# Kernel optimization log

Hardware: AMD Instinct MI355X
Metric: run time of the kernel (lower is better)

## Reference

```python
import jax, jax.numpy as jnp
import numpy as np

K, N, F_IN, F_HID, F_OUT = 4, 8192, 128, 64, 16
DROPOUT_P = 0.3


def setup_inputs() -> dict:
    key = jax.random.key(0)
    ks = jax.random.split(key, 8)
    return {
        "adj": jax.random.uniform(ks[0], (K, N, N), dtype=jnp.float32),
        "x": jax.random.normal(ks[1], (N, F_IN), dtype=jnp.float32),
        "W1": jax.random.normal(ks[2], (F_IN, F_HID), dtype=jnp.float32) * 0.05,
        "b1": jax.random.normal(ks[3], (F_HID,), dtype=jnp.float32) * 0.05,
        "W2": jax.random.normal(ks[4], (F_HID, F_OUT), dtype=jnp.float32) * 0.05,
        "b2": jax.random.normal(ks[5], (F_OUT,), dtype=jnp.float32) * 0.05,
        "pi1": jax.random.normal(ks[6], (K,), dtype=jnp.float32),
        "pi2": jax.random.normal(ks[7], (K,), dtype=jnp.float32),
    }


def _gconv(adj, x, W, b, pi):
    # mixed adjacency: [N, N] = sum_k pi[k] * adj[k]
    A = jnp.einsum('k,knm->nm', pi, adj)
    support = x @ W                     # [N, F_out]
    return A @ support + b              # [N, F_out]


def reference(adj, x, W1, b1, W2, b2, pi1, pi2):
    # gc1.pi is softmax-normalized in Co_GCN.forward
    pi1_n = jax.nn.softmax(pi1)
    h = jax.nn.relu(_gconv(adj, x, W1, b1, pi1_n))   # [N, F_HID]
    # F.dropout with p=0.3, training=True (functional default): fixed-key mask
    keep = jax.random.bernoulli(jax.random.key(42), 1.0 - DROPOUT_P, h.shape)
    h = jnp.where(keep, h / (1.0 - DROPOUT_P), 0.0)
    out = _gconv(adj, h, W2, b2, pi2)                # [N, F_OUT]
    return out
```

## Files before the change

kernel.cpp:

```cpp
#include <hip/hip_runtime.h>
#include <stdint.h>

#define NN 8192
#define FIN 128
#define FH 64
#define FO 16
#define BM 64
#define BN 64
#define SPLIT1 4
#define NRANGE1 (NN / SPLIT1)
#define NCHUNK1 (NRANGE1 / BN)
#define SPLIT2 16
#define NRANGE2 (NN / SPLIT2)

typedef float    f32x4 __attribute__((ext_vector_type(4)));
typedef _Float16 f16x4 __attribute__((ext_vector_type(4)));
typedef _Float16 f16x8 __attribute__((ext_vector_type(8)));
typedef _Float16 h2    __attribute__((ext_vector_type(2)));

union U8 { f16x8 v; h2 p[4]; };

static __device__ __forceinline__ void fma4(float4& acc, float a, const float4 s) {
  acc.x = fmaf(a, s.x, acc.x);
  acc.y = fmaf(a, s.y, acc.y);
  acc.z = fmaf(a, s.z, acc.z);
  acc.w = fmaf(a, s.w, acc.w);
}

static __device__ __forceinline__ float dot2(h2 a, h2 b, float c) {
#if defined(__has_builtin)
#if __has_builtin(__builtin_amdgcn_fdot2)
  return __builtin_amdgcn_fdot2(a, b, c, false);
#else
  return c + (float)a.x * (float)b.x + (float)a.y * (float)b.y;
#endif
#else
  return c + (float)a.x * (float)b.x + (float)a.y * (float)b.y;
#endif
}

__global__ __launch_bounds__(256) void k_s1(const float* __restrict__ x,
                                            const float* __restrict__ W1,
                                            _Float16* __restrict__ S1p) {
  __shared__ float W1l[FIN * FH];
  __shared__ float xl[16][FIN + 4];
  __shared__ float hl[16][FH];
  const int t = threadIdx.x;
  const int n0 = blockIdx.x * 16;
  for (int i = t; i < FIN * FH / 4; i += 256)
    ((float4*)W1l)[i] = ((const float4*)W1)[i];
  for (int i = t; i < 16 * FIN; i += 256) {
    int r = i >> 7, c = i & (FIN - 1);
    xl[r][c] = x[(size_t)(n0 + r) * FIN + c];
  }
  __syncthreads();
  const int m = t >> 4;
  const int j0 = (t & 15) << 2;
  float4 acc = {0.f, 0.f, 0.f, 0.f};
#pragma unroll 8
  for (int k = 0; k < FIN; ++k) {
    float xv = xl[m][k];
    float4 w = *(const float4*)&W1l[k * FH + j0];
    fma4(acc, xv, w);
  }
  *(float4*)&hl[m][j0] = acc;
  __syncthreads();
  const int j = t & 63;
  const int g = t >> 6;
#pragma unroll
  for (int e = 0; e < 2; ++e) {
    const int np = g * 2 + e;
    h2 v;
    v.x = (_Float16)hl[np * 2 + 0][j];
    v.y = (_Float16)hl[np * 2 + 1][j];
    *(h2*)&S1p[(((size_t)(n0 >> 1) + np) * FH + j) * 2] = v;
  }
}

__global__ __launch_bounds__(256) void k_pass1_fused(const float* __restrict__ adj,
                                                     const _Float16* __restrict__ S1p,
                                                     const float* __restrict__ pi1,
                                                     const float* __restrict__ pi2,
                                                     float* __restrict__ hpart,
                                                     _Float16* __restrict__ A2h) {
  __shared__ h2 Alds[BN / 2][BM];
  __shared__ _Float16 S1l[BN / 2][FH][2];
  const int t = threadIdx.x;
  const int mb = blockIdx.x >> 2;
  const int sp = blockIdx.x & 3;

  float p0 = pi1[0], p1 = pi1[1], p2 = pi1[2], p3 = pi1[3];
  float mx = fmaxf(fmaxf(p0, p1), fmaxf(p2, p3));
  float e0 = expf(p0 - mx), e1 = expf(p1 - mx), e2 = expf(p2 - mx), e3 = expf(p3 - mx);
  float inv = 1.0f / (e0 + e1 + e2 + e3);
  const float w0 = e0 * inv, w1 = e1 * inv, w2 = e2 * inv, w3 = e3 * inv;
  const float v0 = pi2[0], v1 = pi2[1], v2 = pi2[2], v3 = pi2[3];

  const size_t NN2 = (size_t)NN * NN;
  const size_t row0 = (size_t)mb * BM;
  const int nbase = sp * NRANGE1;

  const int n4 = t & 15;
  const int ms = t >> 4;
  const int m0 = (t & 15) << 2;
  const int j0 = (t >> 4) << 2;

  f32x4 pf[4][4];
  f16x8 pfS[2];

  float4 acc0 = {0,0,0,0}, acc1 = {0,0,0,0}, acc2 = {0,0,0,0}, acc3 = {0,0,0,0};

  auto ISSUE = [&](int c) {
    const int n0 = nbase + c * BN;
#pragma unroll
    for (int p = 0; p < 4; ++p) {
      const float* g = adj + (row0 + (size_t)(ms + (p << 4))) * NN + (size_t)(n0 + (n4 << 2));
      pf[p][0] = __builtin_nontemporal_load((const f32x4*)g);
      pf[p][1] = __builtin_nontemporal_load((const f32x4*)(g + NN2));
      pf[p][2] = __builtin_nontemporal_load((const f32x4*)(g + 2 * NN2));
      pf[p][3] = __builtin_nontemporal_load((const f32x4*)(g + 3 * NN2));
    }
    const f16x8* src = (const f16x8*)(S1p + (size_t)(n0 >> 1) * FH * 2);
    pfS[0] = src[t];
    pfS[1] = src[t + 256];
  };

  auto STAGE = [&](int c) {
    const int n0 = nbase + c * BN;
#pragma unroll
    for (int p = 0; p < 4; ++p) {
      const int ml = ms + (p << 4);
      f32x4 a0 = pf[p][0], a1 = pf[p][1], a2 = pf[p][2], a3 = pf[p][3];
      float c0 = fmaf(w0, a0.x, fmaf(w1, a1.x, fmaf(w2, a2.x, w3 * a3.x)));
      float c1 = fmaf(w0, a0.y, fmaf(w1, a1.y, fmaf(w2, a2.y, w3 * a3.y)));
      float c2 = fmaf(w0, a0.z, fmaf(w1, a1.z, fmaf(w2, a2.z, w3 * a3.z)));
      float c3 = fmaf(w0, a0.w, fmaf(w1, a1.w, fmaf(w2, a2.w, w3 * a3.w)));
      const int np0 = n4 * 2, np1 = np0 + 1;
      h2 u01; u01.x = (_Float16)c0; u01.y = (_Float16)c1;
      h2 u23; u23.x = (_Float16)c2; u23.y = (_Float16)c3;
      Alds[np0][ml ^ ((np0 & 7) << 2)] = u01;
      Alds[np1][ml ^ ((np1 & 7) << 2)] = u23;
      f16x4 h4;
      h4.x = (_Float16)fmaf(v0, a0.x, fmaf(v1, a1.x, fmaf(v2, a2.x, v3 * a3.x)));
      h4.y = (_Float16)fmaf(v0, a0.y, fmaf(v1, a1.y, fmaf(v2, a2.y, v3 * a3.y)));
      h4.z = (_Float16)fmaf(v0, a0.z, fmaf(v1, a1.z, fmaf(v2, a2.z, v3 * a3.z)));
      h4.w = (_Float16)fmaf(v0, a0.w, fmaf(v1, a1.w, fmaf(v2, a2.w, v3 * a3.w)));
      *(f16x4*)(A2h + (row0 + (size_t)ml) * NN + (size_t)(n0 + (n4 << 2))) = h4;
    }
    f16x8* dst = (f16x8*)&S1l[0][0][0];
    dst[t]       = pfS[0];
    dst[t + 256] = pfS[1];
  };

  ISSUE(0);
  for (int c = 0; c < NCHUNK1; ++c) {
    __syncthreads();
    STAGE(c);
    if (c + 1 < NCHUNK1) ISSUE(c + 1);
    asm volatile("s_waitcnt lgkmcnt(0)" ::: "memory");
    __builtin_amdgcn_s_barrier();
#pragma unroll 4
    for (int np = 0; np < BN / 2; ++np) {
      const int s = (np & 7) << 2;
      U8 a;  a.v  = *(const f16x8*)&Alds[np][m0 ^ s];
      U8 sv; sv.v = *(const f16x8*)&S1l[np][j0][0];
      acc0.x = dot2(a.p[0], sv.p[0], acc0.x);
      acc0.y = dot2(a.p[0], sv.p[1], acc0.y);
      acc0.z = dot2(a.p[0], sv.p[2], acc0.z);
      acc0.w = dot2(a.p[0], sv.p[3], acc0.w);
      acc1.x = dot2(a.p[1], sv.p[0], acc1.x);
      acc1.y = dot2(a.p[1], sv.p[1], acc1.y);
      acc1.z = dot2(a.p[1], sv.p[2], acc1.z);
      acc1.w = dot2(a.p[1], sv.p[3], acc1.w);
      acc2.x = dot2(a.p[2], sv.p[0], acc2.x);
      acc2.y = dot2(a.p[2], sv.p[1], acc2.y);
      acc2.z = dot2(a.p[2], sv.p[2], acc2.z);
      acc2.w = dot2(a.p[2], sv.p[3], acc2.w);
      acc3.x = dot2(a.p[3], sv.p[0], acc3.x);
      acc3.y = dot2(a.p[3], sv.p[1], acc3.y);
      acc3.z = dot2(a.p[3], sv.p[2], acc3.z);
      acc3.w = dot2(a.p[3], sv.p[3], acc3.w);
    }
  }
  float* hp = hpart + (size_t)sp * NN * FH;
  const size_t rbase = (row0 + m0) * FH + j0;
  *(float4*)&hp[rbase]          = acc0;
  *(float4*)&hp[rbase + FH]     = acc1;
  *(float4*)&hp[rbase + 2 * FH] = acc2;
  *(float4*)&hp[rbase + 3 * FH] = acc3;
}

__device__ __forceinline__ float dropout_scale(uint32_t e) {
  uint32_t x0 = 0u;
  uint32_t x1 = e;
  const uint32_t ks1 = 42u;
  const uint32_t ks2 = 0x1BD11BF0u;
  x1 += ks1;
#define TFR(d) { x0 += x1; x1 = (x1 << d) | (x1 >> (32 - d)); x1 ^= x0; }
  TFR(13) TFR(15) TFR(26) TFR(6)   x0 += ks1; x1 += ks2 + 1u;
  TFR(17) TFR(29) TFR(16) TFR(24)  x0 += ks2; x1 += 0u  + 2u;
  TFR(13) TFR(15) TFR(26) TFR(6)   x0 += 0u;  x1 += ks1 + 3u;
  TFR(17) TFR(29) TFR(16) TFR(24)  x0 += ks1; x1 += ks2 + 4u;
  TFR(13) TFR(15) TFR(26) TFR(6)   x0 += ks2; x1 += 0u  + 5u;
#undef TFR
  uint32_t bits = x0 ^ x1;
  float u = __uint_as_float((bits >> 9) | 0x3f800000u) - 1.0f;
  return (u < 0.7f) ? (1.0f / 0.7f) : 0.0f;
}

__global__ __launch_bounds__(256) void k_mid(const float* __restrict__ hpart,
                                             const float* __restrict__ b1,
                                             const float* __restrict__ W2,
                                             _Float16* __restrict__ HWT) {
  __shared__ float hl[4][FH];
  __shared__ float W2l[FH * FO];
  const int t = threadIdx.x;
  const int n0 = blockIdx.x << 2;
  for (int i = t; i < FH * FO; i += 256) W2l[i] = W2[i];
  const int j = t & 63, r = t >> 6;
  const uint32_t idx = (uint32_t)(n0 + r) * FH + j;
  const size_t NF = (size_t)NN * FH;
  float pre = b1[j];
#pragma unroll
  for (int s = 0; s < SPLIT1; ++s) pre += hpart[idx + (size_t)s * NF];
  float v = fmaxf(pre, 0.0f) * dropout_scale(idx);
  hl[r][j] = v;
  __syncthreads();
  if (t < 64) {
    const int rr = t >> 4, f = t & 15;
    float s = 0.f;
#pragma unroll 8
    for (int jj = 0; jj < FH; ++jj)
      s = fmaf(hl[rr][jj], W2l[jj * FO + f], s);
    HWT[(size_t)f * NN + (n0 + rr)] = (_Float16)s;
  }
}

__global__ __launch_bounds__(256) void k_init(const float* __restrict__ b2,
                                              float* __restrict__ out) {
  const int e = blockIdx.x * 256 + threadIdx.x;
  out[e] = b2[e & 15];
}

__global__ __launch_bounds__(64) void k_pass2_dot(const _Float16* __restrict__ A2h,
                                                  const _Float16* __restrict__ HWT,
                                                  float* __restrict__ out) {
  __shared__ f16x8 Htl[64 * 16];
  const int t = threadIdx.x;
  const int mb = blockIdx.x >> 4;
  const int sp = blockIdx.x & 15;
  const size_t row0 = (size_t)mb * BM;
  const int nbase = sp * NRANGE2;

#pragma unroll
  for (int i = 0; i < FO; ++i)
    Htl[t * FO + i] = *(const f16x8*)(HWT + (size_t)i * NN + nbase + t * 8);
  __syncthreads();

  const int fgrp = t & 3;
  const int mgrp = t >> 2;
  const size_t rbase = (row0 + (size_t)mgrp * 4) * NN + nbase;

  float acc[4][4];
#pragma unroll
  for (int j = 0; j < 4; ++j)
#pragma unroll
    for (int i = 0; i < 4; ++i) acc[j][i] = 0.f;

  f16x8 aA[4], aB[4];
#pragma unroll
  for (int j = 0; j < 4; ++j)
    aA[j] = *(const f16x8*)(A2h + rbase + (size_t)j * NN);

  auto LOADB = [&](int o) {
#pragma unroll
    for (int j = 0; j < 4; ++j)
      aB[j] = *(const f16x8*)(A2h + rbase + (size_t)j * NN + o * 8);
  };
  auto LOADA = [&](int o) {
#pragma unroll
    for (int j = 0; j < 4; ++j)
      aA[j] = *(const f16x8*)(A2h + rbase + (size_t)j * NN + o * 8);
  };

  auto COMPUTE = [&](const f16x8* buf, int o) {
    U8 h0, h1, h2v, h3;
    h0.v  = Htl[o * FO + fgrp * 4 + 0];
    h1.v  = Htl[o * FO + fgrp * 4 + 1];
    h2v.v = Htl[o * FO + fgrp * 4 + 2];
    h3.v  = Htl[o * FO + fgrp * 4 + 3];
#pragma unroll
    for (int j = 0; j < 4; ++j) {
      U8 a;
      a.v = buf[j];
#pragma unroll
      for (int q = 0; q < 4; ++q) {
        h2 pa = a.p[q];
        acc[j][0] = dot2(pa, h0.p[q],  acc[j][0]);
        acc[j][1] = dot2(pa, h1.p[q],  acc[j][1]);
        acc[j][2] = dot2(pa, h2v.p[q], acc[j][2]);
        acc[j][3] = dot2(pa, h3.p[q],  acc[j][3]);
      }
    }
  };

  for (int o = 0; o < 64; o += 2) {
    LOADB(o + 1);
    COMPUTE(aA, o);
    if (o + 2 < 64) LOADA(o + 2);
    COMPUTE(aB, o + 1);
  }

#pragma unroll
  for (int j = 0; j < 4; ++j)
#pragma unroll
    for (int i = 0; i < 4; ++i)
      atomicAdd(&out[(row0 + (size_t)mgrp * 4 + j) * FO + fgrp * 4 + i], acc[j][i]);
}

extern "C" void kernel_launch(void* const* d_in, const int* in_sizes, int n_in,
                              void* d_out, int out_size, void* d_ws, size_t ws_size,
                              hipStream_t stream) {
  const float* adj = (const float*)d_in[0];
  const float* x   = (const float*)d_in[1];
  const float* W1  = (const float*)d_in[2];
  const float* b1  = (const float*)d_in[3];
  const float* W2  = (const float*)d_in[4];
  const float* b2  = (const float*)d_in[5];
  const float* pi1 = (const float*)d_in[6];
  const float* pi2 = (const float*)d_in[7];
  float* out = (float*)d_out;
  float* ws  = (float*)d_ws;

  float* hpart  = ws;
  _Float16* S1p = (_Float16*)(hpart + (size_t)SPLIT1 * NN * FH);
  _Float16* A2h = S1p + (size_t)NN * FH;
  _Float16* HWT = A2h + (size_t)NN * NN;

  k_s1         <<<NN / 16,            256, 0, stream>>>(x, W1, S1p);
  k_pass1_fused<<<(NN / BM) * SPLIT1, 256, 0, stream>>>(adj, S1p, pi1, pi2, hpart, A2h);
  k_mid        <<<NN / 4,             256, 0, stream>>>(hpart, b1, W2, HWT);
  k_init       <<<(NN * FO) / 256,    256, 0, stream>>>(b2, out);
  k_pass2_dot  <<<(NN / BM) * SPLIT2,  64, 0, stream>>>(A2h, HWT, out);
}
```

Measured before the change: 337.0 us.

## Double-buffer pass1 adjacency prefetch with smaller chunks and fold init into k_mid

```diff
diff --git a/kernel.cpp b/kernel.cpp
--- a/kernel.cpp
+++ b/kernel.cpp
@@ -6,10 +6,10 @@
 #define FH 64
 #define FO 16
 #define BM 64
-#define BN 64
+#define BN1 32
 #define SPLIT1 4
 #define NRANGE1 (NN / SPLIT1)
-#define NCHUNK1 (NRANGE1 / BN)
+#define NCH1 (NRANGE1 / BN1)
 #define SPLIT2 16
 #define NRANGE2 (NN / SPLIT2)
 
@@ -83,8 +83,8 @@
                                                      const float* __restrict__ pi2,
                                                      float* __restrict__ hpart,
                                                      _Float16* __restrict__ A2h) {
-  __shared__ h2 Alds[BN / 2][BM];
-  __shared__ _Float16 S1l[BN / 2][FH][2];
+  __shared__ h2 Alds[BN1 / 2][BM];
+  __shared__ _Float16 S1l[BN1 / 2][FH][2];
   const int t = threadIdx.x;
   const int mb = blockIdx.x >> 2;
   const int sp = blockIdx.x & 3;
@@ -100,42 +100,40 @@
   const size_t row0 = (size_t)mb * BM;
   const int nbase = sp * NRANGE1;
 
-  const int n4 = t & 15;
-  const int ms = t >> 4;
+  const int q  = t & 7;
+  const int rs = t >> 3;
   const int m0 = (t & 15) << 2;
   const int j0 = (t >> 4) << 2;
 
-  f32x4 pf[4][4];
-  f16x8 pfS[2];
+  f32x4 pfA[2][4], pfB[2][4];
+  f16x8 pfSA, pfSB;
 
   float4 acc0 = {0,0,0,0}, acc1 = {0,0,0,0}, acc2 = {0,0,0,0}, acc3 = {0,0,0,0};
 
-  auto ISSUE = [&](int c) {
-    const int n0 = nbase + c * BN;
-#pragma unroll
-    for (int p = 0; p < 4; ++p) {
-      const float* g = adj + (row0 + (size_t)(ms + (p << 4))) * NN + (size_t)(n0 + (n4 << 2));
+  auto ISSUE = [&](int c, f32x4 (&pf)[2][4], f16x8& pfS) {
+    const int n0 = nbase + c * BN1;
+#pragma unroll
+    for (int p = 0; p < 2; ++p) {
+      const float* g = adj + (row0 + (size_t)(rs + (p << 5))) * NN + (size_t)(n0 + (q << 2));
       pf[p][0] = __builtin_nontemporal_load((const f32x4*)g);
       pf[p][1] = __builtin_nontemporal_load((const f32x4*)(g + NN2));
       pf[p][2] = __builtin_nontemporal_load((const f32x4*)(g + 2 * NN2));
       pf[p][3] = __builtin_nontemporal_load((const f32x4*)(g + 3 * NN2));
     }
-    const f16x8* src = (const f16x8*)(S1p + (size_t)(n0 >> 1) * FH * 2);
-    pfS[0] = src[t];
-    pfS[1] = src[t + 256];
-  };
-
-  auto STAGE = [&](int c) {
-    const int n0 = nbase + c * BN;
-#pragma unroll
-    for (int p = 0; p < 4; ++p) {
-      const int ml = ms + (p << 4);
+    pfS = ((const f16x8*)S1p)[(size_t)(n0 >> 1) * 16 + t];
+  };
+
+  auto STAGE = [&](int c, f32x4 (&pf)[2][4], f16x8& pfS) {
+    const int n0 = nbase + c * BN1;
+#pragma unroll
+    for (int p = 0; p < 2; ++p) {
+      const int ml = rs + (p << 5);
       f32x4 a0 = pf[p][0], a1 = pf[p][1], a2 = pf[p][2], a3 = pf[p][3];
       float c0 = fmaf(w0, a0.x, fmaf(w1, a1.x, fmaf(w2, a2.x, w3 * a3.x)));
       float c1 = fmaf(w0, a0.y, fmaf(w1, a1.y, fmaf(w2, a2.y, w3 * a3.y)));
       float c2 = fmaf(w0, a0.z, fmaf(w1, a1.z, fmaf(w2, a2.z, w3 * a3.z)));
       float c3 = fmaf(w0, a0.w, fmaf(w1, a1.w, fmaf(w2, a2.w, w3 * a3.w)));
-      const int np0 = n4 * 2, np1 = np0 + 1;
+      const int np0 = q << 1, np1 = np0 + 1;
       h2 u01; u01.x = (_Float16)c0; u01.y = (_Float16)c1;
       h2 u23; u23.x = (_Float16)c2; u23.y = (_Float16)c3;
       Alds[np0][ml ^ ((np0 & 7) << 2)] = u01;
@@ -145,22 +143,14 @@
       h4.y = (_Float16)fmaf(v0, a0.y, fmaf(v1, a1.y, fmaf(v2, a2.y, v3 * a3.y)));
       h4.z = (_Float16)fmaf(v0, a0.z, fmaf(v1, a1.z, fmaf(v2, a2.z, v3 * a3.z)));
       h4.w = (_Float16)fmaf(v0, a0.w, fmaf(v1, a1.w, fmaf(v2, a2.w, v3 * a3.w)));
-      *(f16x4*)(A2h + (row0 + (size_t)ml) * NN + (size_t)(n0 + (n4 << 2))) = h4;
+      __builtin_nontemporal_store(h4, (f16x4*)(A2h + (row0 + (size_t)ml) * NN + (size_t)(n0 + (q << 2))));
     }
-    f16x8* dst = (f16x8*)&S1l[0][0][0];
-    dst[t]       = pfS[0];
-    dst[t + 256] = pfS[1];
-  };
-
-  ISSUE(0);
-  for (int c = 0; c < NCHUNK1; ++c) {
-    __syncthreads();
-    STAGE(c);
-    if (c + 1 < NCHUNK1) ISSUE(c + 1);
-    asm volatile("s_waitcnt lgkmcnt(0)" ::: "memory");
-    __builtin_amdgcn_s_barrier();
+    ((f16x8*)&S1l[0][0][0])[t] = pfS;
+  };
+
+  auto COMPUTE = [&]() {
 #pragma unroll 4
-    for (int np = 0; np < BN / 2; ++np) {
+    for (int np = 0; np < BN1 / 2; ++np) {
       const int s = (np & 7) << 2;
       U8 a;  a.v  = *(const f16x8*)&Alds[np][m0 ^ s];
       U8 sv; sv.v = *(const f16x8*)&S1l[np][j0][0];
@@ -181,7 +171,27 @@
       acc3.z = dot2(a.p[3], sv.p[2], acc3.z);
       acc3.w = dot2(a.p[3], sv.p[3], acc3.w);
     }
-  }
+  };
+
+  ISSUE(0, pfA, pfSA);
+  ISSUE(1, pfB, pfSB);
+  for (int c = 0; c < NCH1; c += 2) {
+    asm volatile("" ::: "memory");
+    __builtin_amdgcn_s_barrier();
+    STAGE(c, pfA, pfSA);
+    if (c + 2 < NCH1) ISSUE(c + 2, pfA, pfSA);
+    asm volatile("s_waitcnt lgkmcnt(0)" ::: "memory");
+    __builtin_amdgcn_s_barrier();
+    COMPUTE();
+    asm volatile("" ::: "memory");
+    __builtin_amdgcn_s_barrier();
+    STAGE(c + 1, pfB, pfSB);
+    if (c + 3 < NCH1) ISSUE(c + 3, pfB, pfSB);
+    asm volatile("s_waitcnt lgkmcnt(0)" ::: "memory");
+    __builtin_amdgcn_s_barrier();
+    COMPUTE();
+  }
+
   float* hp = hpart + (size_t)sp * NN * FH;
   const size_t rbase = (row0 + m0) * FH + j0;
   *(float4*)&hp[rbase]          = acc0;
@@ -211,10 +221,14 @@
 __global__ __launch_bounds__(256) void k_mid(const float* __restrict__ hpart,
                                              const float* __restrict__ b1,
                                              const float* __restrict__ W2,
-                                             _Float16* __restrict__ HWT) {
+                                             const float* __restrict__ b2,
+                                             _Float16* __restrict__ HWT,
+                                             float* __restrict__ out) {
   __shared__ float hl[4][FH];
   __shared__ float W2l[FH * FO];
   const int t = threadIdx.x;
+  if (blockIdx.x < (NN * FO) / 256)
+    out[blockIdx.x * 256 + t] = b2[t & 15];
   const int n0 = blockIdx.x << 2;
   for (int i = t; i < FH * FO; i += 256) W2l[i] = W2[i];
   const int j = t & 63, r = t >> 6;
@@ -234,12 +248,6 @@
       s = fmaf(hl[rr][jj], W2l[jj * FO + f], s);
     HWT[(size_t)f * NN + (n0 + rr)] = (_Float16)s;
   }
-}
-
-__global__ __launch_bounds__(256) void k_init(const float* __restrict__ b2,
-                                              float* __restrict__ out) {
-  const int e = blockIdx.x * 256 + threadIdx.x;
-  out[e] = b2[e & 15];
 }
 
 __global__ __launch_bounds__(64) void k_pass2_dot(const _Float16* __restrict__ A2h,
@@ -339,7 +347,6 @@
 
   k_s1         <<<NN / 16,            256, 0, stream>>>(x, W1, S1p);
   k_pass1_fused<<<(NN / BM) * SPLIT1, 256, 0, stream>>>(adj, S1p, pi1, pi2, hpart, A2h);
-  k_mid        <<<NN / 4,             256, 0, stream>>>(hpart, b1, W2, HWT);
-  k_init       <<<(NN * FO) / 256,    256, 0, stream>>>(b2, out);
+  k_mid        <<<NN / 4,             256, 0, stream>>>(hpart, b1, W2, b2, HWT, out);
   k_pass2_dot  <<<(NN / BM) * SPLIT2,  64, 0, stream>>>(A2h, HWT, out);
 }
```

New measurement: 407.4 us. +20.9%, slower.
